# Optimization experiments

Measured on AMD Instinct MI355X. Metric: run time of the kernel, lower is better.

Reference implementation:

```python
import jax, jax.numpy as jnp
import numpy as np

VOCAB, DIM = 100000, 300
B, L = 4096, 200
HIDDEN, OUT = 1000, 3


def setup_inputs() -> dict:
    key = jax.random.key(0)
    k_emb, k_x, k_len, k_w1, k_b1, k_w2, k_b2 = jax.random.split(key, 7)
    emb_table = jax.random.normal(k_emb, (VOCAB, DIM), dtype=jnp.float32)
    x = jax.random.randint(k_x, (B, L), 0, VOCAB)
    lengths = jax.random.randint(k_len, (B,), 1, L + 1)  # >=1 to avoid div-by-zero
    W1 = jax.random.normal(k_w1, (2 * DIM, HIDDEN), dtype=jnp.float32) * 0.02
    b1 = jax.random.normal(k_b1, (HIDDEN,), dtype=jnp.float32) * 0.02
    W2 = jax.random.normal(k_w2, (HIDDEN, OUT), dtype=jnp.float32) * 0.02
    b2 = jax.random.normal(k_b2, (OUT,), dtype=jnp.float32) * 0.02
    return {"emb_table": emb_table, "W1": W1, "b1": b1, "W2": W2, "b2": b2,
            "x": x, "lengths": lengths}


def reference(emb_table, W1, b1, W2, b2, x, lengths):
    emb = emb_table[x]                                   # [B, L, D] gather
    # Faithful to original: mean uses sum over ALL positions (incl. padding)
    mean_pooled = jnp.sum(emb, axis=1) / lengths[:, None].astype(emb.dtype)  # [B, D]
    # Max only over the first `length` real tokens
    mask = jnp.arange(L)[None, :] < lengths[:, None]     # [B, L]
    neg_inf = jnp.array(-jnp.inf, dtype=emb.dtype)
    max_pooled = jnp.max(jnp.where(mask[:, :, None], emb, neg_inf), axis=1)  # [B, D]
    rep = jnp.concatenate([mean_pooled, max_pooled], axis=1)  # [B, 2D]
    h = jax.nn.relu(rep @ W1 + b1)                       # [B, 1000]
    return h @ W2 + b2                                   # [B, OUT]
```

## Files before the change

### kernel.cpp

```cpp
#include <hip/hip_runtime.h>
#include <math.h>

#define VOCAB  100000
#define DIM    300
#define IDIM   320
#define BB     4096
#define LL     200
#define HIDDEN 1000
#define OUTC   3
#define KT     19
#define NT     64
#define MTILES (BB / 16)

#define QSCALE (6.0f / 127.0f)
#define QINV   (127.0f / 6.0f)

#define W1_BLKS   ((KT * NT * 64 + 255) / 256)
#define INIT_BLKS ((BB * OUTC + 255) / 256)
#define CONV_BLKS ((VOCAB * 20 + 255) / 256)

typedef __attribute__((ext_vector_type(8))) short  short8;
typedef __attribute__((ext_vector_type(4))) float  floatx4;
typedef __attribute__((ext_vector_type(2))) unsigned short ushort2v;

__device__ inline ushort f2bf(float f) {
    union { float f; unsigned u; } v; v.f = f;
    unsigned u = v.u;
    u += 0x7fffu + ((u >> 16) & 1u);
    return (ushort)(u >> 16);
}
__device__ inline float4 f4max(float4 a, float4 b) {
    return make_float4(fmaxf(a.x, b.x), fmaxf(a.y, b.y), fmaxf(a.z, b.z), fmaxf(a.w, b.w));
}
__device__ inline float4 f4add(float4 a, float4 b) {
    return make_float4(a.x + b.x, a.y + b.y, a.z + b.z, a.w + b.w);
}
__device__ inline unsigned pkmax16(unsigned a, unsigned b) {
    union { unsigned u; ushort2v v; } x, y, r;
    x.u = a; y.u = b;
    r.v = __builtin_elementwise_max(x.v, y.v);
    return r.u;
}

__device__ inline int a_slot(int k, int ml) {
    const int kt = k >> 5, kk = k & 31;
    return ((kt << 6) + ml + ((kk >> 3) << 4)) * 8 + (kk & 7);
}

__device__ inline unsigned q4(float a, float b, float c, float d) {
    int q0 = min(max(__float2int_rn(a * QINV) + 128, 0), 255);
    int q1 = min(max(__float2int_rn(b * QINV) + 128, 0), 255);
    int q2 = min(max(__float2int_rn(c * QINV) + 128, 0), 255);
    int q3 = min(max(__float2int_rn(d * QINV) + 128, 0), 255);
    return (unsigned)q0 | ((unsigned)q1 << 8) | ((unsigned)q2 << 16) | ((unsigned)q3 << 24);
}

__global__ __launch_bounds__(256) void prep_all(
    const float* __restrict__ emb, unsigned char* __restrict__ embQ,
    const float* __restrict__ W1,  ushort* __restrict__ w1p,
    const float* __restrict__ b2,  float* __restrict__ out)
{
    const int bid = blockIdx.x;
    const int tid = threadIdx.x;
    if (bid < W1_BLKS) {
        const int g = bid * 256 + tid;
        if (g >= KT * NT * 64) return;
        const int lane = g & 63;
        const int nt   = (g >> 6) & (NT - 1);
        const int kt   = g >> 12;
        const int n    = nt * 16 + (lane & 15);
        const int kb   = kt * 32 + ((lane >> 4) << 3);
        short8 v;
        #pragma unroll
        for (int j = 0; j < 8; ++j) {
            const int k = kb + j;
            const float f = (k < 600 && n < HIDDEN) ? W1[k * HIDDEN + n] : 0.f;
            v[j] = (short)f2bf(f);
        }
        ((short8*)w1p)[g] = v;
    } else if (bid < W1_BLKS + INIT_BLKS) {
        const int g = (bid - W1_BLKS) * 256 + tid;
        if (g < BB * OUTC) out[g] = b2[g % OUTC];
    } else {
        const int g = (bid - W1_BLKS - INIT_BLKS) * 256 + tid;
        if (g >= VOCAB * 20) return;
        const int row = g / 20;
        const int c   = g - row * 20;
        const float4* rp = (const float4*)(emb + (size_t)row * DIM);
        uint4 o;
        unsigned* ow = (unsigned*)&o;
        #pragma unroll
        for (int v = 0; v < 4; ++v) {
            const int fi = 4 * c + v;
            float4 f = (fi < 75) ? rp[fi] : make_float4(0.f, 0.f, 0.f, 0.f);
            ow[v] = q4(f.x, f.y, f.z, f.w);
        }
        *(uint4*)(embQ + (size_t)g * 16) = o;
    }
}

__global__ __launch_bounds__(256, 8) void gather_pool_i8(
    const unsigned char* __restrict__ embQ,
    const int*           __restrict__ x,
    const int*           __restrict__ lengths,
    ushort*              __restrict__ repA)
{
    __shared__ int      xS[LL];
    __shared__ unsigned pS[3][20][8];
    __shared__ unsigned pM[3][20][8];

    const int tid  = threadIdx.x;
    const int lane = tid & 63;
    const int wave = tid >> 6;
    const int row  = blockIdx.x;

    for (int i = tid; i < LL; i += 256) xS[i] = x[row * LL + i];
    const int len = lengths[row];
    __syncthreads();

    const int  t0   = wave * 50;
    const int  vmax = min(max(len - t0, 0), 50);
    const bool ga   = (lane < 20);
    const bool ld   = (lane < 40);
    const int  lg   = ga ? lane : (lane - 20);

    unsigned sLo[4], sHi[4], mLo[4], mHi[4];
    #pragma unroll
    for (int w = 0; w < 4; ++w) { sLo[w] = sHi[w] = 0u; mLo[w] = mHi[w] = 0u; }

    uint4 raw = make_uint4(0, 0, 0, 0);
    const int full = vmax >> 1;
    int p = 0;
    for (; p < full; ++p) {
        const int tA  = t0 + 2 * p;
        const int idx = ga ? xS[tA] : xS[tA + 1];
        if (ld) raw = *(const uint4*)(embQ + (size_t)idx * IDIM + 16 * lg);
        const unsigned* ww = (const unsigned*)&raw;
        #pragma unroll
        for (int w = 0; w < 4; ++w) {
            const unsigned u  = ww[w];
            const unsigned lo = u & 0x00FF00FFu;
            const unsigned hi = (u >> 8) & 0x00FF00FFu;
            sLo[w] += lo;  sHi[w] += hi;
            mLo[w] = pkmax16(mLo[w], lo);
            mHi[w] = pkmax16(mHi[w], hi);
        }
    }
    if (vmax & 1) {
        const int tA  = t0 + 2 * p;
        const int idx = ga ? xS[tA] : xS[tA + 1];
        if (ld) raw = *(const uint4*)(embQ + (size_t)idx * IDIM + 16 * lg);
        const unsigned* ww = (const unsigned*)&raw;
        #pragma unroll
        for (int w = 0; w < 4; ++w) {
            const unsigned u  = ww[w];
            const unsigned lo = u & 0x00FF00FFu;
            const unsigned hi = (u >> 8) & 0x00FF00FFu;
            sLo[w] += lo;  sHi[w] += hi;
            if (ga) {
                mLo[w] = pkmax16(mLo[w], lo);
                mHi[w] = pkmax16(mHi[w], hi);
            }
        }
        ++p;
    }
    for (; p < 25; ++p) {
        const int tA  = t0 + 2 * p;
        const int idx = ga ? xS[tA] : xS[tA + 1];
        if (ld) raw = *(const uint4*)(embQ + (size_t)idx * IDIM + 16 * lg);
        const unsigned* ww = (const unsigned*)&raw;
        #pragma unroll
        for (int w = 0; w < 4; ++w) {
            const unsigned u = ww[w];
            sLo[w] += u & 0x00FF00FFu;
            sHi[w] += (u >> 8) & 0x00FF00FFu;
        }
    }

    {
        const int src = ga ? (lane + 20) : lane;
        #pragma unroll
        for (int w = 0; w < 4; ++w) {
            sLo[w] += (unsigned)__shfl((int)sLo[w], src);
            sHi[w] += (unsigned)__shfl((int)sHi[w], src);
            mLo[w] = pkmax16(mLo[w], (unsigned)__shfl((int)mLo[w], src));
            mHi[w] = pkmax16(mHi[w], (unsigned)__shfl((int)mHi[w], src));
        }
    }

    if (wave != 0 && ga) {
        #pragma unroll
        for (int w = 0; w < 4; ++w) {
            pS[wave - 1][lane][w]     = sLo[w];
            pS[wave - 1][lane][4 + w] = sHi[w];
            pM[wave - 1][lane][w]     = mLo[w];
            pM[wave - 1][lane][4 + w] = mHi[w];
        }
    }
    __syncthreads();
    if (wave == 0 && ga) {
        #pragma unroll
        for (int wv = 0; wv < 3; ++wv)
            #pragma unroll
            for (int w = 0; w < 4; ++w) {
                sLo[w] += pS[wv][lane][w];
                sHi[w] += pS[wv][lane][4 + w];
                mLo[w] = pkmax16(mLo[w], pM[wv][lane][w]);
                mHi[w] = pkmax16(mHi[w], pM[wv][lane][4 + w]);
            }

        float s[16], m[16];
        #pragma unroll
        for (int w = 0; w < 4; ++w) {
            s[4*w+0] = (float)(sLo[w] & 0xFFFFu);
            s[4*w+2] = (float)(sLo[w] >> 16);
            s[4*w+1] = (float)(sHi[w] & 0xFFFFu);
            s[4*w+3] = (float)(sHi[w] >> 16);
            m[4*w+0] = (float)(mLo[w] & 0xFFFFu);
            m[4*w+2] = (float)(mLo[w] >> 16);
            m[4*w+1] = (float)(mHi[w] & 0xFFFFu);
            m[4*w+3] = (float)(mHi[w] >> 16);
        }

        const float c1 = QSCALE / (float)len;
        const int mt = row >> 4;
        const int ml = row & 15;
        ushort* rb = repA + (size_t)mt * (KT * 512);

        ushort mv[16];
        #pragma unroll
        for (int j = 0; j < 16; ++j) mv[j] = f2bf((m[j] - 128.f) * QSCALE);

        if (lane < 18) {
            #pragma unroll
            for (int h = 0; h < 2; ++h) {
                short8 q;
                #pragma unroll
                for (int j = 0; j < 8; ++j)
                    q[j] = (short)f2bf((s[8*h + j] - 25600.f) * c1);
                *(short8*)(rb + a_slot(16 * lane + 8 * h, ml)) = q;
            }
            #pragma unroll
            for (int h = 0; h < 2; ++h) {
                const int k0 = 300 + 16 * lane + 8 * h;
                *(ushort4*)(rb + a_slot(k0, ml)) =
                    make_ushort4(mv[8*h+0], mv[8*h+1], mv[8*h+2], mv[8*h+3]);
                *(ushort4*)(rb + a_slot(k0 + 4, ml)) =
                    make_ushort4(mv[8*h+4], mv[8*h+5], mv[8*h+6], mv[8*h+7]);
            }
        } else if (lane == 18) {
            short8 q;
            #pragma unroll
            for (int j = 0; j < 8; ++j) q[j] = (short)f2bf((s[j] - 25600.f) * c1);
            *(short8*)(rb + a_slot(288, ml)) = q;
            *(ushort4*)(rb + a_slot(296, ml)) =
                make_ushort4(f2bf((s[8] - 25600.f) * c1), f2bf((s[9] - 25600.f) * c1),
                             f2bf((s[10] - 25600.f) * c1), f2bf((s[11] - 25600.f) * c1));
            *(ushort4*)(rb + a_slot(588, ml)) = make_ushort4(mv[0], mv[1], mv[2], mv[3]);
            *(ushort4*)(rb + a_slot(592, ml)) = make_ushort4(mv[4], mv[5], mv[6], mv[7]);
            *(ushort4*)(rb + a_slot(596, ml)) = make_ushort4(mv[8], mv[9], mv[10], mv[11]);
            *(ushort4*)(rb + a_slot(600, ml)) = make_ushort4(0, 0, 0, 0);
        } else {
            *(ushort4*)(rb + a_slot(604, ml)) = make_ushort4(0, 0, 0, 0);
        }
    }
}

__global__ __launch_bounds__(256, 8) void gather_pool_f32(
    const float* __restrict__ emb,
    const int*   __restrict__ x,
    const int*   __restrict__ lengths,
    ushort*      __restrict__ repA)
{
    __shared__ int    xS[LL];
    __shared__ float4 pS[3][75];
    __shared__ float4 pM[3][75];

    const int tid  = threadIdx.x;
    const int lane = tid & 63;
    const int wave = tid >> 6;
    const int row  = blockIdx.x;

    for (int i = tid; i < LL; i += 256) xS[i] = x[row * LL + i];
    const int len = lengths[row];
    __syncthreads();

    const int  t0   = wave * (LL / 4);
    const int  vmax = min(max(len - t0, 0), LL / 4);
    const bool tl   = (lane < 11);
    const float4 z4 = make_float4(0.f, 0.f, 0.f, 0.f);

    float4 s4 = z4, st = z4;
    float4 m4 = make_float4(-INFINITY, -INFINITY, -INFINITY, -INFINITY);
    float4 mt = m4;

    int t = 0;
    #pragma unroll 4
    for (; t < vmax; ++t) {
        const int idx = xS[t0 + t];
        const float4* rp = (const float4*)(emb + (size_t)idx * DIM);
        float4 a = rp[lane];
        float4 b = tl ? rp[64 + lane] : z4;
        s4 = f4add(s4, a); st = f4add(st, b);
        m4 = f4max(m4, a); mt = f4max(mt, b);
    }
    #pragma unroll 4
    for (; t < LL / 4; ++t) {
        const int idx = xS[t0 + t];
        const float4* rp = (const float4*)(emb + (size_t)idx * DIM);
        float4 a = rp[lane];
        float4 b = tl ? rp[64 + lane] : z4;
        s4 = f4add(s4, a); st = f4add(st, b);
    }

    if (wave != 0) {
        pS[wave - 1][lane] = s4; pM[wave - 1][lane] = m4;
        if (tl) { pS[wave - 1][64 + lane] = st; pM[wave - 1][64 + lane] = mt; }
    }
    __syncthreads();
    if (wave == 0) {
        #pragma unroll
        for (int w = 0; w < 3; ++w) {
            s4 = f4add(s4, pS[w][lane]); m4 = f4max(m4, pM[w][lane]);
            if (tl) { st = f4add(st, pS[w][64 + lane]); mt = f4max(mt, pM[w][64 + lane]); }
        }
        const float inv = 1.0f / (float)len;
        const int mtile = row >> 4;
        const int ml    = row & 15;
        ushort* rb = repA + (size_t)mtile * (KT * 512);
        {
            ushort4 q = make_ushort4(f2bf(s4.x*inv), f2bf(s4.y*inv), f2bf(s4.z*inv), f2bf(s4.w*inv));
            *(ushort4*)(rb + a_slot(4 * lane, ml)) = q;
        }
        {
            ushort4 q = make_ushort4(f2bf(m4.x), f2bf(m4.y), f2bf(m4.z), f2bf(m4.w));
            *(ushort4*)(rb + a_slot(300 + 4 * lane, ml)) = q;
        }
        if (tl) {
            ushort4 q1 = make_ushort4(f2bf(st.x*inv), f2bf(st.y*inv), f2bf(st.z*inv), f2bf(st.w*inv));
            *(ushort4*)(rb + a_slot(256 + 4 * lane, ml)) = q1;
            ushort4 q2 = make_ushort4(f2bf(mt.x), f2bf(mt.y), f2bf(mt.z), f2bf(mt.w));
            *(ushort4*)(rb + a_slot(556 + 4 * lane, ml)) = q2;
        }
        if (lane >= 56) rb[a_slot(600 + (lane - 56), ml)] = 0;
    }
}

__global__ __launch_bounds__(256, 4) void mlp_mfma(
    const ushort* __restrict__ w1p,
    const ushort* __restrict__ repA,
    const float*  __restrict__ b1,
    const float*  __restrict__ W2,
    float*        __restrict__ out)
{
    __shared__ short8 aS[KT * 64];
    __shared__ float  red[4][16][3];

    const int tid  = threadIdx.x;
    const int lane = tid & 63;
    const int wave = tid >> 6;
    const int mt   = blockIdx.x >> 2;
    const int q    = blockIdx.x & 3;

    {
        const short8* ap = (const short8*)(repA + (size_t)mt * (KT * 512));
        for (int i = tid; i < KT * 64; i += 256) aS[i] = ap[i];
    }
    __syncthreads();

    const int nt0 = q * 16 + wave * 4;
    const short8* bp = (const short8*)w1p;

    floatx4 acc[4];
    #pragma unroll
    for (int s = 0; s < 4; ++s) acc[s] = (floatx4){0.f, 0.f, 0.f, 0.f};

    #pragma unroll
    for (int kt = 0; kt < KT; ++kt) {
        const short8 av = aS[kt * 64 + lane];
        const short8 b0 = bp[(kt * NT + nt0 + 0) * 64 + lane];
        const short8 b1v = bp[(kt * NT + nt0 + 1) * 64 + lane];
        const short8 b2v = bp[(kt * NT + nt0 + 2) * 64 + lane];
        const short8 b3 = bp[(kt * NT + nt0 + 3) * 64 + lane];
        acc[0] = __builtin_amdgcn_mfma_f32_16x16x32_bf16(av, b0,  acc[0], 0, 0, 0);
        acc[1] = __builtin_amdgcn_mfma_f32_16x16x32_bf16(av, b1v, acc[1], 0, 0, 0);
        acc[2] = __builtin_amdgcn_mfma_f32_16x16x32_bf16(av, b2v, acc[2], 0, 0, 0);
        acc[3] = __builtin_amdgcn_mfma_f32_16x16x32_bf16(av, b3,  acc[3], 0, 0, 0);
    }

    float po[4][3];
    #pragma unroll
    for (int rg = 0; rg < 4; ++rg)
        #pragma unroll
        for (int j = 0; j < OUTC; ++j) po[rg][j] = 0.f;

    #pragma unroll
    for (int s = 0; s < 4; ++s) {
        const int n = (nt0 + s) * 16 + (lane & 15);
        const bool valid = (n < HIDDEN);
        const float bb  = b1[valid ? n : 0];
        const float w20 = valid ? W2[n * 3 + 0] : 0.f;
        const float w21 = valid ? W2[n * 3 + 1] : 0.f;
        const float w22 = valid ? W2[n * 3 + 2] : 0.f;
        #pragma unroll
        for (int rg = 0; rg < 4; ++rg) {
            const float h = fmaxf(acc[s][rg] + bb, 0.f);
            po[rg][0] = fmaf(h, w20, po[rg][0]);
            po[rg][1] = fmaf(h, w21, po[rg][1]);
            po[rg][2] = fmaf(h, w22, po[rg][2]);
        }
    }

    #pragma unroll
    for (int rg = 0; rg < 4; ++rg) {
        #pragma unroll
        for (int j = 0; j < OUTC; ++j) {
            float v = po[rg][j];
            v += __shfl_xor(v, 1);
            v += __shfl_xor(v, 2);
            v += __shfl_xor(v, 4);
            v += __shfl_xor(v, 8);
            if ((lane & 15) == 0) red[wave][(lane >> 4) * 4 + rg][j] = v;
        }
    }
    __syncthreads();

    if (tid < 16 * OUTC) {
        const int m = tid / OUTC, j = tid % OUTC;
        const float s = red[0][m][j] + red[1][m][j] + red[2][m][j] + red[3][m][j];
        atomicAdd(&out[(size_t)(mt * 16 + m) * OUTC + j], s);
    }
}

extern "C" void kernel_launch(void* const* d_in, const int* in_sizes, int n_in,
                              void* d_out, int out_size, void* d_ws, size_t ws_size,
                              hipStream_t stream) {
    const float* emb = (const float*)d_in[0];
    const float* W1  = (const float*)d_in[1];
    const float* b1  = (const float*)d_in[2];
    const float* W2  = (const float*)d_in[3];
    const float* b2  = (const float*)d_in[4];
    const int*   x   = (const int*)d_in[5];
    const int*   len = (const int*)d_in[6];
    float* out = (float*)d_out;

    const size_t W1P_ELTS  = (size_t)KT * NT * 64 * 8;
    const size_t REPA_ELTS = (size_t)MTILES * KT * 512;
    ushort* w1p  = (ushort*)d_ws;
    ushort* repA = w1p + W1P_ELTS;
    unsigned char* embQ = (unsigned char*)(repA + REPA_ELTS);
    const size_t need = (W1P_ELTS + REPA_ELTS) * 2 + (size_t)VOCAB * IDIM;
    const bool doConv = (ws_size >= need);

    const int prepGrid = W1_BLKS + INIT_BLKS + (doConv ? CONV_BLKS : 0);
    hipLaunchKernelGGL(prep_all, dim3(prepGrid), dim3(256), 0, stream,
                       emb, embQ, W1, w1p, b2, out);
    if (doConv) {
        hipLaunchKernelGGL(gather_pool_i8, dim3(BB), dim3(256), 0, stream,
                           embQ, x, len, repA);
    } else {
        hipLaunchKernelGGL(gather_pool_f32, dim3(BB), dim3(256), 0, stream,
                           emb, x, len, repA);
    }
    hipLaunchKernelGGL(mlp_mfma, dim3(MTILES * 4), dim3(256), 0, stream,
                       w1p, repA, b1, W2, out);
}
```

Measured before the change: 256.0 us.

## Unroll gather loop by two and retile MLP to 2x2 MFMA blocks

The int8 gather-pool loop now issues two embedding row loads per iteration so more memory requests are in flight. The MLP kernel switches from one 16-row M tile with four N tiles per wave to two M tiles with two N tiles per wave. Each B fragment is then reused across two A rows, which halves W1 global reads per output, while the grid keeps the same block count. The shared A buffer doubles in size and is reused for the reduction scratch, which may reduce occupancy slightly.

```diff
diff --git a/kernel.cpp b/kernel.cpp
--- a/kernel.cpp
+++ b/kernel.cpp
@@ -53,6 +53,29 @@
     int q2 = min(max(__float2int_rn(c * QINV) + 128, 0), 255);
     int q3 = min(max(__float2int_rn(d * QINV) + 128, 0), 255);
     return (unsigned)q0 | ((unsigned)q1 << 8) | ((unsigned)q2 << 16) | ((unsigned)q3 << 24);
+}
+
+__device__ inline void acc_sm(const uint4& raw, unsigned* sLo, unsigned* sHi,
+                              unsigned* mLo, unsigned* mHi) {
+    const unsigned* ww = (const unsigned*)&raw;
+    #pragma unroll
+    for (int w = 0; w < 4; ++w) {
+        const unsigned u  = ww[w];
+        const unsigned lo = u & 0x00FF00FFu;
+        const unsigned hi = (u >> 8) & 0x00FF00FFu;
+        sLo[w] += lo;  sHi[w] += hi;
+        mLo[w] = pkmax16(mLo[w], lo);
+        mHi[w] = pkmax16(mHi[w], hi);
+    }
+}
+__device__ inline void acc_s(const uint4& raw, unsigned* sLo, unsigned* sHi) {
+    const unsigned* ww = (const unsigned*)&raw;
+    #pragma unroll
+    for (int w = 0; w < 4; ++w) {
+        const unsigned u = ww[w];
+        sLo[w] += u & 0x00FF00FFu;
+        sHi[w] += (u >> 8) & 0x00FF00FFu;
+    }
 }
 
 __global__ __launch_bounds__(256) void prep_all(
@@ -123,58 +146,68 @@
     const bool ga   = (lane < 20);
     const bool ld   = (lane < 40);
     const int  lg   = ga ? lane : (lane - 20);
+    const unsigned char* base = embQ + 16 * lg;
 
     unsigned sLo[4], sHi[4], mLo[4], mHi[4];
     #pragma unroll
     for (int w = 0; w < 4; ++w) { sLo[w] = sHi[w] = 0u; mLo[w] = mHi[w] = 0u; }
 
-    uint4 raw = make_uint4(0, 0, 0, 0);
     const int full = vmax >> 1;
     int p = 0;
-    for (; p < full; ++p) {
-        const int tA  = t0 + 2 * p;
-        const int idx = ga ? xS[tA] : xS[tA + 1];
-        if (ld) raw = *(const uint4*)(embQ + (size_t)idx * IDIM + 16 * lg);
-        const unsigned* ww = (const unsigned*)&raw;
+    for (; p + 2 <= full; p += 2) {
+        const int tA = t0 + 2 * p;
+        const int i0 = ga ? xS[tA]     : xS[tA + 1];
+        const int i1 = ga ? xS[tA + 2] : xS[tA + 3];
+        uint4 r0 = make_uint4(0,0,0,0), r1 = make_uint4(0,0,0,0);
+        if (ld) {
+            r0 = *(const uint4*)(base + (size_t)i0 * IDIM);
+            r1 = *(const uint4*)(base + (size_t)i1 * IDIM);
+        }
+        acc_sm(r0, sLo, sHi, mLo, mHi);
+        acc_sm(r1, sLo, sHi, mLo, mHi);
+    }
+    if (p < full) {
+        const int tA = t0 + 2 * p;
+        const int i0 = ga ? xS[tA] : xS[tA + 1];
+        uint4 r0 = make_uint4(0,0,0,0);
+        if (ld) r0 = *(const uint4*)(base + (size_t)i0 * IDIM);
+        acc_sm(r0, sLo, sHi, mLo, mHi);
+        ++p;
+    }
+    if (vmax & 1) {
+        const int tA = t0 + 2 * p;
+        const int i0 = ga ? xS[tA] : xS[tA + 1];
+        uint4 r0 = make_uint4(0,0,0,0);
+        if (ld) r0 = *(const uint4*)(base + (size_t)i0 * IDIM);
+        const unsigned* ww = (const unsigned*)&r0;
         #pragma unroll
         for (int w = 0; w < 4; ++w) {
             const unsigned u  = ww[w];
             const unsigned lo = u & 0x00FF00FFu;
             const unsigned hi = (u >> 8) & 0x00FF00FFu;
             sLo[w] += lo;  sHi[w] += hi;
-            mLo[w] = pkmax16(mLo[w], lo);
-            mHi[w] = pkmax16(mHi[w], hi);
-        }
-    }
-    if (vmax & 1) {
-        const int tA  = t0 + 2 * p;
-        const int idx = ga ? xS[tA] : xS[tA + 1];
-        if (ld) raw = *(const uint4*)(embQ + (size_t)idx * IDIM + 16 * lg);
-        const unsigned* ww = (const unsigned*)&raw;
-        #pragma unroll
-        for (int w = 0; w < 4; ++w) {
-            const unsigned u  = ww[w];
-            const unsigned lo = u & 0x00FF00FFu;
-            const unsigned hi = (u >> 8) & 0x00FF00FFu;
-            sLo[w] += lo;  sHi[w] += hi;
-            if (ga) {
-                mLo[w] = pkmax16(mLo[w], lo);
-                mHi[w] = pkmax16(mHi[w], hi);
-            }
+            if (ga) { mLo[w] = pkmax16(mLo[w], lo); mHi[w] = pkmax16(mHi[w], hi); }
         }
         ++p;
     }
-    for (; p < 25; ++p) {
-        const int tA  = t0 + 2 * p;
-        const int idx = ga ? xS[tA] : xS[tA + 1];
-        if (ld) raw = *(const uint4*)(embQ + (size_t)idx * IDIM + 16 * lg);
-        const unsigned* ww = (const unsigned*)&raw;
-        #pragma unroll
-        for (int w = 0; w < 4; ++w) {
-            const unsigned u = ww[w];
-            sLo[w] += u & 0x00FF00FFu;
-            sHi[w] += (u >> 8) & 0x00FF00FFu;
-        }
+    for (; p + 2 <= 25; p += 2) {
+        const int tA = t0 + 2 * p;
+        const int i0 = ga ? xS[tA]     : xS[tA + 1];
+        const int i1 = ga ? xS[tA + 2] : xS[tA + 3];
+        uint4 r0 = make_uint4(0,0,0,0), r1 = make_uint4(0,0,0,0);
+        if (ld) {
+            r0 = *(const uint4*)(base + (size_t)i0 * IDIM);
+            r1 = *(const uint4*)(base + (size_t)i1 * IDIM);
+        }
+        acc_s(r0, sLo, sHi);
+        acc_s(r1, sLo, sHi);
+    }
+    if (p < 25) {
+        const int tA = t0 + 2 * p;
+        const int i0 = ga ? xS[tA] : xS[tA + 1];
+        uint4 r0 = make_uint4(0,0,0,0);
+        if (ld) r0 = *(const uint4*)(base + (size_t)i0 * IDIM);
+        acc_s(r0, sLo, sHi);
     }
 
     {
@@ -349,86 +382,96 @@
 __global__ __launch_bounds__(256, 4) void mlp_mfma(
     const ushort* __restrict__ w1p,
     const ushort* __restrict__ repA,
-    const float*  __restrict__ b1,
+    const float*  __restrict__ bias1,
     const float*  __restrict__ W2,
     float*        __restrict__ out)
 {
-    __shared__ short8 aS[KT * 64];
-    __shared__ float  red[4][16][3];
+    __shared__ short8 aS[2 * KT * 64];
 
     const int tid  = threadIdx.x;
     const int lane = tid & 63;
     const int wave = tid >> 6;
-    const int mt   = blockIdx.x >> 2;
-    const int q    = blockIdx.x & 3;
+    const int mp   = blockIdx.x >> 3;
+    const int e    = blockIdx.x & 7;
 
     {
-        const short8* ap = (const short8*)(repA + (size_t)mt * (KT * 512));
-        for (int i = tid; i < KT * 64; i += 256) aS[i] = ap[i];
-    }
-    __syncthreads();
-
-    const int nt0 = q * 16 + wave * 4;
+        const short8* ap = (const short8*)(repA + (size_t)(2 * mp) * (KT * 512));
+        for (int i = tid; i < 2 * KT * 64; i += 256) aS[i] = ap[i];
+    }
+    __syncthreads();
+
+    const int nt0 = e * 8 + wave;
+    const int nt1 = nt0 + 4;
     const short8* bp = (const short8*)w1p;
 
-    floatx4 acc[4];
-    #pragma unroll
-    for (int s = 0; s < 4; ++s) acc[s] = (floatx4){0.f, 0.f, 0.f, 0.f};
+    floatx4 acc[2][2];
+    #pragma unroll
+    for (int mi = 0; mi < 2; ++mi)
+        #pragma unroll
+        for (int s = 0; s < 2; ++s) acc[mi][s] = (floatx4){0.f, 0.f, 0.f, 0.f};
 
     #pragma unroll
     for (int kt = 0; kt < KT; ++kt) {
-        const short8 av = aS[kt * 64 + lane];
-        const short8 b0 = bp[(kt * NT + nt0 + 0) * 64 + lane];
-        const short8 b1v = bp[(kt * NT + nt0 + 1) * 64 + lane];
-        const short8 b2v = bp[(kt * NT + nt0 + 2) * 64 + lane];
-        const short8 b3 = bp[(kt * NT + nt0 + 3) * 64 + lane];
-        acc[0] = __builtin_amdgcn_mfma_f32_16x16x32_bf16(av, b0,  acc[0], 0, 0, 0);
-        acc[1] = __builtin_amdgcn_mfma_f32_16x16x32_bf16(av, b1v, acc[1], 0, 0, 0);
-        acc[2] = __builtin_amdgcn_mfma_f32_16x16x32_bf16(av, b2v, acc[2], 0, 0, 0);
-        acc[3] = __builtin_amdgcn_mfma_f32_16x16x32_bf16(av, b3,  acc[3], 0, 0, 0);
-    }
-
-    float po[4][3];
-    #pragma unroll
-    for (int rg = 0; rg < 4; ++rg)
-        #pragma unroll
-        for (int j = 0; j < OUTC; ++j) po[rg][j] = 0.f;
-
-    #pragma unroll
-    for (int s = 0; s < 4; ++s) {
-        const int n = (nt0 + s) * 16 + (lane & 15);
+        const short8 av0 = aS[kt * 64 + lane];
+        const short8 av1 = aS[KT * 64 + kt * 64 + lane];
+        const short8 bv0 = bp[(kt * NT + nt0) * 64 + lane];
+        const short8 bv1 = bp[(kt * NT + nt1) * 64 + lane];
+        acc[0][0] = __builtin_amdgcn_mfma_f32_16x16x32_bf16(av0, bv0, acc[0][0], 0, 0, 0);
+        acc[0][1] = __builtin_amdgcn_mfma_f32_16x16x32_bf16(av0, bv1, acc[0][1], 0, 0, 0);
+        acc[1][0] = __builtin_amdgcn_mfma_f32_16x16x32_bf16(av1, bv0, acc[1][0], 0, 0, 0);
+        acc[1][1] = __builtin_amdgcn_mfma_f32_16x16x32_bf16(av1, bv1, acc[1][1], 0, 0, 0);
+    }
+    __syncthreads();
+    float* red = (float*)aS;
+
+    float po[2][4][3];
+    #pragma unroll
+    for (int mi = 0; mi < 2; ++mi)
+        #pragma unroll
+        for (int rg = 0; rg < 4; ++rg)
+            #pragma unroll
+            for (int j = 0; j < OUTC; ++j) po[mi][rg][j] = 0.f;
+
+    #pragma unroll
+    for (int s = 0; s < 2; ++s) {
+        const int n = (s ? nt1 : nt0) * 16 + (lane & 15);
         const bool valid = (n < HIDDEN);
-        const float bb  = b1[valid ? n : 0];
+        const float bb  = bias1[valid ? n : 0];
         const float w20 = valid ? W2[n * 3 + 0] : 0.f;
         const float w21 = valid ? W2[n * 3 + 1] : 0.f;
         const float w22 = valid ? W2[n * 3 + 2] : 0.f;
         #pragma unroll
-        for (int rg = 0; rg < 4; ++rg) {
-            const float h = fmaxf(acc[s][rg] + bb, 0.f);
-            po[rg][0] = fmaf(h, w20, po[rg][0]);
-            po[rg][1] = fmaf(h, w21, po[rg][1]);
-            po[rg][2] = fmaf(h, w22, po[rg][2]);
-        }
-    }
-
-    #pragma unroll
-    for (int rg = 0; rg < 4; ++rg) {
-        #pragma unroll
-        for (int j = 0; j < OUTC; ++j) {
-            float v = po[rg][j];
-            v += __shfl_xor(v, 1);
-            v += __shfl_xor(v, 2);
-            v += __shfl_xor(v, 4);
-            v += __shfl_xor(v, 8);
-            if ((lane & 15) == 0) red[wave][(lane >> 4) * 4 + rg][j] = v;
-        }
-    }
-    __syncthreads();
-
-    if (tid < 16 * OUTC) {
+        for (int mi = 0; mi < 2; ++mi)
+            #pragma unroll
+            for (int rg = 0; rg < 4; ++rg) {
+                const float h = fmaxf(acc[mi][s][rg] + bb, 0.f);
+                po[mi][rg][0] = fmaf(h, w20, po[mi][rg][0]);
+                po[mi][rg][1] = fmaf(h, w21, po[mi][rg][1]);
+                po[mi][rg][2] = fmaf(h, w22, po[mi][rg][2]);
+            }
+    }
+
+    #pragma unroll
+    for (int mi = 0; mi < 2; ++mi)
+        #pragma unroll
+        for (int rg = 0; rg < 4; ++rg)
+            #pragma unroll
+            for (int j = 0; j < OUTC; ++j) {
+                float v = po[mi][rg][j];
+                v += __shfl_xor(v, 1);
+                v += __shfl_xor(v, 2);
+                v += __shfl_xor(v, 4);
+                v += __shfl_xor(v, 8);
+                if ((lane & 15) == 0)
+                    red[(wave * 32 + mi * 16 + (lane >> 4) * 4 + rg) * 3 + j] = v;
+            }
+    __syncthreads();
+
+    if (tid < 32 * OUTC) {
         const int m = tid / OUTC, j = tid % OUTC;
-        const float s = red[0][m][j] + red[1][m][j] + red[2][m][j] + red[3][m][j];
-        atomicAdd(&out[(size_t)(mt * 16 + m) * OUTC + j], s);
+        const float s = red[(0 * 32 + m) * 3 + j] + red[(1 * 32 + m) * 3 + j]
+                      + red[(2 * 32 + m) * 3 + j] + red[(3 * 32 + m) * 3 + j];
+        atomicAdd(&out[(size_t)(mp * 32 + m) * OUTC + j], s);
     }
 }
 
@@ -462,6 +505,6 @@
         hipLaunchKernelGGL(gather_pool_f32, dim3(BB), dim3(256), 0, stream,
                            emb, x, len, repA);
     }
-    hipLaunchKernelGGL(mlp_mfma, dim3(MTILES * 4), dim3(256), 0, stream,
+    hipLaunchKernelGGL(mlp_mfma, dim3((MTILES / 2) * 8), dim3(256), 0, stream,
                        w1p, repA, b1, W2, out);
 }
```

Measured after the change: 256.9 us. About the same (+0.3%).
